# Performance work log

Measured on AMD Instinct MI355X. Metric: run time of the kernel, lower is better.

## Reference

```python
import jax, jax.numpy as jnp
import numpy as np

Q = 32          # latent position dim; state vs = [v, s] has dim 2Q
N = 131072      # batch of ODE states
H = 50          # BNN hidden width (n_hidden=50 in source)
STEPS = 16      # fixed-step Euler steps (dense time grid)
DT = 0.1        # dt default from forward()
LN_EPS = 1e-5


def setup_inputs() -> dict:
    key = jax.random.key(0)
    ks = jax.random.split(key, 6)
    d = 2 * Q
    # weights scaled by 1/sqrt(fan_in) so Euler integration stays stable
    return {
        "z0": jax.random.normal(ks[0], (N, d), jnp.float32),
        "logp0": jax.random.normal(ks[1], (N,), jnp.float32),
        "W1": jax.random.normal(ks[2], (d, H), jnp.float32) / np.sqrt(d).astype(np.float32),
        "b1": jnp.zeros((H,), jnp.float32),
        "g1": jnp.ones((H,), jnp.float32),
        "be1": jnp.zeros((H,), jnp.float32),
        "W2": jax.random.normal(ks[3], (H, H), jnp.float32) / np.sqrt(H).astype(np.float32),
        "b2": jnp.zeros((H,), jnp.float32),
        "g2": jnp.ones((H,), jnp.float32),
        "be2": jnp.zeros((H,), jnp.float32),
        "W3": jax.random.normal(ks[4], (H, Q), jnp.float32) / np.sqrt(H).astype(np.float32),
        "b3": jnp.zeros((Q,), jnp.float32),
    }


def _layernorm(x, g, b):
    m = jnp.mean(x, axis=-1, keepdims=True)
    v = jnp.mean((x - m) ** 2, axis=-1, keepdims=True)
    return (x - m) * jax.lax.rsqrt(v + LN_EPS) * g + b


def reference(z0, logp0, W1, b1, g1, be1, W2, b2, g2, be2, W3, b3):
    d = z0.shape[1]
    q = d // 2

    def f(vs):  # BNN dynamics: [N, 2q] -> [N, q]
        h = jax.nn.celu(_layernorm(vs @ W1 + b1, g1, be1))
        h = jax.nn.celu(_layernorm(h @ W2 + b2, g2, be2))
        return h @ W3 + b3

    basis = jnp.eye(q, d, dtype=z0.dtype)  # [q, 2q] unit tangents in the velocity block

    def rhs(vs):
        dv = f(vs)          # dv/dt = f(vs)
        ds = vs[:, :q]      # ds/dt = v
        dvs = jnp.concatenate([dv, ds], axis=1)
        # trace of d(dv)/d(v) via q forward-mode JVPs (fused analogue of the
        # per-dim torch.autograd.grad loop in ode2vae_rhs)
        def jvp_i(e):
            _, t = jax.jvp(f, (vs,), (jnp.broadcast_to(e, vs.shape),))
            return t  # [N, q]
        tang = jax.vmap(jvp_i)(basis)        # [q, N, q]
        tr = jnp.einsum("ini->n", tang)      # sum_i d(dv_i)/d(v_i)
        return dvs, -tr

    def step(carry, _):
        vs, lp = carry
        dvs, dlp = rhs(vs)
        vs2 = vs + DT * dvs
        lp2 = lp + DT * dlp
        return (vs2, lp2), (vs2, lp2)

    _, (zt, lp) = jax.lax.scan(step, (z0, logp0), None, length=STEPS)
    # [STEPS, N, 2q+1]: trajectory states with log-density appended
    return jnp.concatenate([zt, lp[..., None]], axis=-1)
```

## Files before the change

kernel.cpp:

```cpp
#include <hip/hip_runtime.h>
#include <hip/hip_fp16.h>

#define NPART 131072
#define QDIM 32
#define DDIM 64
#define HDIM 50
#define STEPS 16
#define DT 0.1f
#define LN_EPS 1e-5f
#define INV_H 0.02f
#define ODIM 65

#define WS_W1TH 0
#define WS_W2TH 1600
#define WS_UTH  3000
#define WS_MH   4400
#define WS_W3H  5800
#define WS_JV   6600
#define WS_HV   6800
#define WS_TOT  7000

#define LT_W2TH 0
#define LT_UTH  1400
#define LT_TOT  2800

#define SLOT_FLOATS (HDIM * 256)
#define LDS_FLOATS  (SLOT_FLOATS + LT_TOT)

typedef float f4a __attribute__((ext_vector_type(4)));
typedef float f4u __attribute__((ext_vector_type(4), aligned(4)));
typedef unsigned int u32;
typedef _Float16 h2f __attribute__((ext_vector_type(2)));

__device__ __forceinline__ h2f as_h2(u32 x) { h2f r; __builtin_memcpy(&r, &x, 4); return r; }
__device__ __forceinline__ u32 h2bits(float a, float b) {
    h2f p; p[0] = (_Float16)a; p[1] = (_Float16)b;
    u32 r; __builtin_memcpy(&r, &p, 4); return r;
}
__device__ __forceinline__ h2f mk_h2(float a, float b) {
    h2f p; p[0] = (_Float16)a; p[1] = (_Float16)b; return p;
}

#if __has_builtin(__builtin_amdgcn_fdot2)
#define FDOT2(a, b, c) __builtin_amdgcn_fdot2((a), (b), (c), false)
#else
#define FDOT2(a, b, c) ((float)(a)[0] * (float)(b)[0] + ((float)(a)[1] * (float)(b)[1] + (c)))
#endif

__global__ void ode2vae_setup(const float* __restrict__ W1,
                              const float* __restrict__ W2,
                              const float* __restrict__ W3,
                              const float* __restrict__ b1, const float* __restrict__ g1,
                              const float* __restrict__ be1,
                              const float* __restrict__ b2, const float* __restrict__ g2,
                              const float* __restrict__ be2,
                              float* __restrict__ ws)
{
    const int tid = threadIdx.x;
    u32* wsu = (u32*)ws;
    for (int i = tid; i < WS_TOT; i += 256) wsu[i] = 0u;
    __syncthreads();
    for (int idx = tid; idx < HDIM * 32; idx += 256) {
        const int h = idx / 32, k = idx % 32;
        wsu[WS_W1TH + h * 32 + k] = h2bits(W1[(2 * k) * HDIM + h], W1[(2 * k + 1) * HDIM + h]);
    }
    for (int idx = tid; idx < HDIM * 25; idx += 256) {
        const int j = idx / 25, k = idx % 25;
        float w2p[2], up[2], mp[2];
        #pragma unroll
        for (int s_ = 0; s_ < 2; ++s_) {
            const int h = 2 * k + s_;
            float u = 0.f;
            #pragma unroll
            for (int i = 0; i < QDIM; ++i)
                u = fmaf(W1[i * HDIM + h], W3[j * QDIM + i], u);
            const float w2 = W2[h * HDIM + j];
            float rs = 0.f;
            for (int jj = 0; jj < HDIM; ++jj) rs += W2[h * HDIM + jj];
            w2p[s_] = w2; up[s_] = u; mp[s_] = u * (w2 - INV_H * rs);
        }
        wsu[WS_W2TH + j * 28 + k] = h2bits(w2p[0], w2p[1]);
        wsu[WS_UTH  + j * 28 + k] = h2bits(up[0], up[1]);
        wsu[WS_MH   + j * 28 + k] = h2bits(mp[0], mp[1]);
    }
    for (int idx = tid; idx < HDIM * 16; idx += 256) {
        const int j = idx / 16, k = idx % 16;
        wsu[WS_W3H + j * 16 + k] = h2bits(W3[j * QDIM + 2 * k], W3[j * QDIM + 2 * k + 1]);
    }
    if (tid < HDIM) {
        float acc = 0.f;
        #pragma unroll
        for (int i = 0; i < QDIM; ++i) {
            float rs1 = 0.f;
            for (int h = 0; h < HDIM; ++h) rs1 += W1[i * HDIM + h];
            acc = fmaf(rs1, W3[tid * QDIM + i], acc);
        }
        ws[WS_JV + tid * 4 + 0] = g2[tid];
        ws[WS_JV + tid * 4 + 1] = be2[tid];
        ws[WS_JV + tid * 4 + 2] = b2[tid];
        ws[WS_JV + tid * 4 + 3] = acc;
        ws[WS_HV + tid * 4 + 0] = b1[tid];
        ws[WS_HV + tid * 4 + 1] = g1[tid];
        ws[WS_HV + tid * 4 + 2] = be1[tid];
        ws[WS_HV + tid * 4 + 3] = 0.f;
    }
}

#define DOT64(res, rowp, P)                                           \
    {                                                                 \
        float q0 = 0.f, q1 = 0.f, q2 = 0.f, q3 = 0.f;                 \
        const uint4* R_ = (const uint4*)(rowp);                       \
        _Pragma("unroll")                                             \
        for (int c_ = 0; c_ < 8; ++c_) {                              \
            const uint4 u_ = R_[c_];                                  \
            q0 = FDOT2(as_h2(u_.x), (P)[4*c_ + 0], q0);               \
            q1 = FDOT2(as_h2(u_.y), (P)[4*c_ + 1], q1);               \
            q2 = FDOT2(as_h2(u_.z), (P)[4*c_ + 2], q2);               \
            q3 = FDOT2(as_h2(u_.w), (P)[4*c_ + 3], q3);               \
        }                                                             \
        res = (q0 + q1) + (q2 + q3);                                  \
    }
#define DOT56(res, rowp, P)                                           \
    {                                                                 \
        float q0 = 0.f, q1 = 0.f, q2 = 0.f, q3 = 0.f;                 \
        const uint4* R_ = (const uint4*)(rowp);                       \
        _Pragma("unroll")                                             \
        for (int c_ = 0; c_ < 7; ++c_) {                              \
            const uint4 u_ = R_[c_];                                  \
            q0 = FDOT2(as_h2(u_.x), (P)[4*c_ + 0], q0);               \
            q1 = FDOT2(as_h2(u_.y), (P)[4*c_ + 1], q1);               \
            q2 = FDOT2(as_h2(u_.z), (P)[4*c_ + 2], q2);               \
            q3 = FDOT2(as_h2(u_.w), (P)[4*c_ + 3], q3);               \
        }                                                             \
        res = (q0 + q1) + (q2 + q3);                                  \
    }

#define LDROW7(RB, SRC) { const uint4* S_ = (const uint4*)(SRC);      \
    _Pragma("unroll") for (int c_ = 0; c_ < 7; ++c_) RB[c_] = S_[c_]; }
#define LDROW4(RB, SRC) { const uint4* S_ = (const uint4*)(SRC);      \
    _Pragma("unroll") for (int c_ = 0; c_ < 4; ++c_) RB[c_] = S_[c_]; }

#define PKDOT_RB(res, RB, P)                                          \
    {                                                                 \
        h2f a0 = mk_h2(0.f, 0.f), a1_ = a0;                           \
        _Pragma("unroll")                                             \
        for (int c_ = 0; c_ < 7; ++c_) {                              \
            a0  = as_h2(RB[c_].x) * (P)[4*c_ + 0] + a0;               \
            a1_ = as_h2(RB[c_].y) * (P)[4*c_ + 1] + a1_;              \
            a0  = as_h2(RB[c_].z) * (P)[4*c_ + 2] + a0;               \
            a1_ = as_h2(RB[c_].w) * (P)[4*c_ + 3] + a1_;              \
        }                                                             \
        a0 = a0 + a1_;                                                \
        res = (float)a0[0] + (float)a0[1];                            \
    }

#define PKDOT_SAX_RB(res, RB, PA, ys, D)                              \
    {                                                                 \
        h2f a0 = mk_h2(0.f, 0.f), a1_ = a0;                           \
        _Pragma("unroll")                                             \
        for (int c_ = 0; c_ < 7; ++c_) {                              \
            const h2f x_ = as_h2(RB[c_].x), y_ = as_h2(RB[c_].y);     \
            const h2f z_ = as_h2(RB[c_].z), w_ = as_h2(RB[c_].w);     \
            a0  = x_ * (PA)[4*c_ + 0] + a0;                           \
            (D)[4*c_ + 0] = x_ * (ys) + (D)[4*c_ + 0];                \
            a1_ = y_ * (PA)[4*c_ + 1] + a1_;                          \
            (D)[4*c_ + 1] = y_ * (ys) + (D)[4*c_ + 1];                \
            a0  = z_ * (PA)[4*c_ + 2] + a0;                           \
            (D)[4*c_ + 2] = z_ * (ys) + (D)[4*c_ + 2];                \
            a1_ = w_ * (PA)[4*c_ + 3] + a1_;                          \
            (D)[4*c_ + 3] = w_ * (ys) + (D)[4*c_ + 3];                \
        }                                                             \
        a0 = a0 + a1_;                                                \
        res = (float)a0[0] + (float)a0[1];                            \
    }

#define PK2DOT_SAX_RB(rA, rB, RB, PA, PB, xs, D)                      \
    {                                                                 \
        h2f aA = mk_h2(0.f, 0.f), aB = aA;                            \
        _Pragma("unroll")                                             \
        for (int c_ = 0; c_ < 7; ++c_) {                              \
            const h2f x_ = as_h2(RB[c_].x), y_ = as_h2(RB[c_].y);     \
            const h2f z_ = as_h2(RB[c_].z), w_ = as_h2(RB[c_].w);     \
            aA = x_ * (PA)[4*c_ + 0] + aA;                            \
            aB = x_ * (PB)[4*c_ + 0] + aB;                            \
            (D)[4*c_ + 0] = x_ * (xs) + (D)[4*c_ + 0];                \
            aA = y_ * (PA)[4*c_ + 1] + aA;                            \
            aB = y_ * (PB)[4*c_ + 1] + aB;                            \
            (D)[4*c_ + 1] = y_ * (xs) + (D)[4*c_ + 1];                \
            aA = z_ * (PA)[4*c_ + 2] + aA;                            \
            aB = z_ * (PB)[4*c_ + 2] + aB;                            \
            (D)[4*c_ + 2] = z_ * (xs) + (D)[4*c_ + 2];                \
            aA = w_ * (PA)[4*c_ + 3] + aA;                            \
            aB = w_ * (PB)[4*c_ + 3] + aB;                            \
            (D)[4*c_ + 3] = w_ * (xs) + (D)[4*c_ + 3];                \
        }                                                             \
        rA = (float)aA[0] + (float)aA[1];                             \
        rB = (float)aB[0] + (float)aB[1];                             \
    }

#define SAXPY_RB4(RB, sh, D)                                          \
    {                                                                 \
        _Pragma("unroll")                                             \
        for (int c_ = 0; c_ < 4; ++c_) {                              \
            (D)[4*c_ + 0] = as_h2(RB[c_].x) * (sh) + (D)[4*c_ + 0];   \
            (D)[4*c_ + 1] = as_h2(RB[c_].y) * (sh) + (D)[4*c_ + 1];   \
            (D)[4*c_ + 2] = as_h2(RB[c_].z) * (sh) + (D)[4*c_ + 2];   \
            (D)[4*c_ + 3] = as_h2(RB[c_].w) * (sh) + (D)[4*c_ + 3];   \
        }                                                             \
    }

__global__ __launch_bounds__(256, 2)
void ode2vae_main(const float* __restrict__ z0, const float* __restrict__ logp0,
                  const float* __restrict__ b3,
                  const float* __restrict__ wsc,
                  float* out)
{
    __shared__ float lds[LDS_FLOATS];
    const int tid = threadIdx.x;
    const int n = blockIdx.x * 256 + tid;

    {
        const u32* src = (const u32*)wsc;
        u32* dst = (u32*)(lds + SLOT_FLOATS);
        for (int i = tid; i < 1400; i += 256) dst[LT_W2TH + i] = src[WS_W2TH + i];
        for (int i = tid; i < 1400; i += 256) dst[LT_UTH + i]  = src[WS_UTH + i];
    }
    __syncthreads();

    float* const L = lds + tid;
    const u32* LW2TH = (const u32*)(lds + SLOT_FLOATS) + LT_W2TH;
    const u32* LUTH  = (const u32*)(lds + SLOT_FLOATS) + LT_UTH;
    const u32* GW1TH = (const u32*)wsc + WS_W1TH;
    const u32* GMH   = (const u32*)wsc + WS_MH;
    const u32* GW3H  = (const u32*)wsc + WS_W3H;
    const f4a* GJV   = (const f4a*)(wsc + WS_JV);
    const f4a* GHV   = (const f4a*)(wsc + WS_HV);

    float lp = logp0[n];
    const float* const zrow0 = z0 + (size_t)n * DDIM;

    for (int s = 0; s < STEPS; ++s) {
        float* const odst = out + ((size_t)s * NPART + (size_t)n) * ODIM;
        const float* const zprev = (s == 0) ? zrow0
            : (out + ((size_t)(s - 1) * NPART + (size_t)n) * ODIM);

        float zq[QDIM], zs[QDIM];
        #pragma unroll
        for (int k = 0; k < 8; ++k) {
            f4u v = *(const f4u*)(zprev + 4 * k);
            zq[4*k] = v[0]; zq[4*k+1] = v[1]; zq[4*k+2] = v[2]; zq[4*k+3] = v[3];
        }
        #pragma unroll
        for (int k = 0; k < 8; ++k) {
            f4u v = *(const f4u*)(zprev + QDIM + 4 * k);
            zs[4*k] = v[0]; zs[4*k+1] = v[1]; zs[4*k+2] = v[2]; zs[4*k+3] = v[3];
        }
        h2f zp[32];
        #pragma unroll
        for (int k = 0; k < 16; ++k) zp[k] = mk_h2(zq[2*k], zq[2*k+1]);
        #pragma unroll
        for (int k = 0; k < 16; ++k) zp[16 + k] = mk_h2(zs[2*k], zs[2*k+1]);

        float m1a = 0.f, v1a = 0.f;
        #pragma unroll 1
        for (int h = 0; h < HDIM; ++h) {
            float a1h;
            DOT64(a1h, GW1TH + h * 32, zp);
            const f4a hv = GHV[h];
            a1h += hv[0];
            L[h * 256] = a1h;
            m1a += a1h;
            v1a = fmaf(a1h, a1h, v1a);
        }
        #pragma unroll
        for (int k = 0; k < QDIM; ++k) zs[k] = fmaf(DT, zq[k], zs[k]);
        #pragma unroll
        for (int k = 0; k < 8; ++k) {
            f4u v = {zs[4*k], zs[4*k+1], zs[4*k+2], zs[4*k+3]};
            *(f4u*)(odst + QDIM + 4 * k) = v;
        }
        const float m1 = m1a * INV_H;
        float var1 = v1a * INV_H - m1 * m1;
        var1 = var1 > 0.f ? var1 : 0.f;
        const float r1 = rsqrtf(var1 + LN_EPS);

        h2f xh1p[28], hhp[28], w1vp[28], w1xp[28];
        #pragma unroll
        for (int hp = 0; hp < 25; ++hp) {
            const float xa = (L[(2*hp) * 256] - m1) * r1;
            const float xb = (L[(2*hp + 1) * 256] - m1) * r1;
            const f4a hva = GHV[2*hp], hvb = GHV[2*hp + 1];
            const float ya = fmaf(xa, hva[1], hva[2]);
            const float yb = fmaf(xb, hvb[1], hvb[2]);
            const float ea = __expf(ya), eb = __expf(yb);
            const float ca = (ya > 0.f) ? ya : (ea - 1.f);
            const float cb = (yb > 0.f) ? yb : (eb - 1.f);
            const float wa = ((ya > 0.f) ? 1.f : ea) * (hva[1] * r1);
            const float wb = ((yb > 0.f) ? 1.f : eb) * (hvb[1] * r1);
            xh1p[hp] = mk_h2(xa, xb);
            hhp[hp]  = mk_h2(ca, cb);
            w1vp[hp] = mk_h2(wa, wb);
            w1xp[hp] = mk_h2(wa * xa, wb * xb);
        }
        #pragma unroll
        for (int hp = 25; hp < 28; ++hp) {
            xh1p[hp] = mk_h2(0.f, 0.f); hhp[hp] = mk_h2(0.f, 0.f);
            w1vp[hp] = mk_h2(0.f, 0.f); w1xp[hp] = mk_h2(0.f, 0.f);
        }

        float m2a = 0.f, v2a = 0.f;
        #pragma unroll 1
        for (int j = 0; j < HDIM; ++j) {
            float a2j;
            DOT56(a2j, LW2TH + j * 28, hhp);
            const f4a jv = GJV[j];
            a2j += jv[2];
            L[j * 256] = a2j;
            m2a += a2j;
            v2a = fmaf(a2j, a2j, v2a);
        }
        const float m2 = m2a * INV_H;
        float var2 = v2a * INV_H - m2 * m2;
        var2 = var2 > 0.f ? var2 : 0.f;
        const float r2 = rsqrtf(var2 + LN_EPS);

        h2f duyp[28], php[28];
        #pragma unroll
        for (int k = 0; k < 28; ++k) { duyp[k] = mk_h2(0.f, 0.f); php[k] = mk_h2(0.f, 0.f); }
        h2f dvp[16];
        #pragma unroll
        for (int k = 0; k < 16; ++k) dvp[k] = mk_h2(0.f, 0.f);
        float suA = 0.f, syA = 0.f, tuA = 0.f, tyA = 0.f;
        float A2a = 0.f, A2b = 0.f, A2c = 0.f;
        float A3a = 0.f, A3b = 0.f, A3c = 0.f;
        float T1A = 0.f;
        #pragma unroll 1
        for (int j = 0; j < HDIM; ++j) {
            const float x2 = (L[j * 256] - m2) * r2;
            const f4a jv = GJV[j];
            const float y = fmaf(x2, jv[0], jv[1]);
            const float e = __expf(y);
            const float w2vj = ((y > 0.f) ? 1.f : e) * (jv[0] * r2);
            const float h2v = (y > 0.f) ? y : (e - 1.f);

            uint4 RU[7];
            LDROW7(RU, LUTH + j * 28);
            const float y3 = x2 * w2vj;
            const h2f y3h = mk_h2(y3, y3);
            float t;
            PKDOT_SAX_RB(t, RU, xh1p, y3h, duyp);

            uint4 RW[7];
            LDROW7(RW, LW2TH + j * 28);
            const h2f x2h = mk_h2(x2, x2);
            float cS2, cS3;
            PK2DOT_SAX_RB(cS2, cS3, RW, w1vp, w1xp, x2h, php);

            uint4 RM[7];
            LDROW7(RM, GMH + j * 28);
            float cTA;
            PKDOT_RB(cTA, RM, w1vp);

            uint4 R3[4];
            LDROW4(R3, GW3H + j * 16);
            const h2f hb = mk_h2(h2v, h2v);
            SAXPY_RB4(R3, hb, dvp);

            const float svw = jv[3] * w2vj;
            const float tw  = w2vj * t;
            suA += svw; syA = fmaf(svw, x2, syA);
            tuA += tw;  tyA = fmaf(tw, x2, tyA);
            A2a = fmaf(svw, cS2, A2a); A2b += cS2; A2c = fmaf(x2, cS2, A2c);
            A3a = fmaf(tw,  cS3, A3a); A3b += cS3; A3c = fmaf(x2, cS3, A3c);
            T1A = fmaf(w2vj, cTA, T1A);
        }

        float zq2[QDIM];
        #pragma unroll
        for (int k = 0; k < 8; ++k) {
            f4u v = *(const f4u*)(zprev + 4 * k);
            zq2[4*k] = v[0]; zq2[4*k+1] = v[1]; zq2[4*k+2] = v[2]; zq2[4*k+3] = v[3];
        }

        const float suH = suA * INV_H, syH = syA * INV_H;
        const float tuH = tuA * INV_H, tyH = tyA * INV_H;
        const float S2 = A2a - suH * A2b - syH * A2c;
        const float S3 = A3a - tuH * A3b - tyH * A3c;
        float T1c;
        {
            h2f acc0 = mk_h2(0.f, 0.f), acc1 = acc0;
            #pragma unroll
            for (int k = 0; k < 28; k += 2) {
                acc0 = (w1vp[k] * duyp[k]) * php[k] + acc0;
                acc1 = (w1vp[k+1] * duyp[k+1]) * php[k+1] + acc1;
            }
            acc0 = acc0 + acc1;
            T1c = (float)acc0[0] + (float)acc0[1];
        }
        const float tr = T1A - (T1c + S2 + S3) * INV_H;

        lp = fmaf(-DT, tr, lp);
        #pragma unroll
        for (int k = 0; k < 16; ++k) {
            const float da = (float)dvp[k][0] + b3[2*k];
            const float db = (float)dvp[k][1] + b3[2*k + 1];
            zq2[2*k]     = fmaf(DT, da, zq2[2*k]);
            zq2[2*k + 1] = fmaf(DT, db, zq2[2*k + 1]);
        }
        #pragma unroll
        for (int k = 0; k < 8; ++k) {
            f4u v = {zq2[4*k], zq2[4*k+1], zq2[4*k+2], zq2[4*k+3]};
            *(f4u*)(odst + 4 * k) = v;
        }
        odst[DDIM] = lp;
    }
}

extern "C" void kernel_launch(void* const* d_in, const int* in_sizes, int n_in,
                              void* d_out, int out_size, void* d_ws, size_t ws_size,
                              hipStream_t stream)
{
    const float* z0    = (const float*)d_in[0];
    const float* logp0 = (const float*)d_in[1];
    const float* W1    = (const float*)d_in[2];
    const float* b1    = (const float*)d_in[3];
    const float* g1    = (const float*)d_in[4];
    const float* be1   = (const float*)d_in[5];
    const float* W2    = (const float*)d_in[6];
    const float* b2    = (const float*)d_in[7];
    const float* g2    = (const float*)d_in[8];
    const float* be2   = (const float*)d_in[9];
    const float* W3    = (const float*)d_in[10];
    const float* b3    = (const float*)d_in[11];
    float* out = (float*)d_out;
    float* ws  = (float*)d_ws;

    hipLaunchKernelGGL(ode2vae_setup, dim3(1), dim3(256), 0, stream,
                       W1, W2, W3, b1, g1, be1, b2, g2, be2, ws);
    hipLaunchKernelGGL(ode2vae_main, dim3(NPART / 256), dim3(256), 0, stream,
                       z0, logp0, b3, ws, out);
}
```

Before: 1.347 ms.

## Pack per-thread LDS activations to fp16 pairs and move U matrix to global

The per-thread LDS scratch for layer activations now stores two fp16 values per 32-bit slot, halving its footprint. The U weight matrix is read from global (cached) memory instead of LDS, leaving only W2 in shared memory. The hidden loops are unrolled by two to match the packed layout. Less LDS per block can allow more resident blocks, but rounding pre-LayerNorm activations to fp16 loses precision and adds extra global or cache traffic for U.

```diff
diff --git a/kernel.cpp b/kernel.cpp
--- a/kernel.cpp
+++ b/kernel.cpp
@@ -20,12 +20,9 @@
 #define WS_HV   6800
 #define WS_TOT  7000
 
-#define LT_W2TH 0
-#define LT_UTH  1400
-#define LT_TOT  2800
-
-#define SLOT_FLOATS (HDIM * 256)
-#define LDS_FLOATS  (SLOT_FLOATS + LT_TOT)
+#define SLOT_U32   (25 * 256)
+#define LT_W2TH    SLOT_U32
+#define LDS_U32    (SLOT_U32 + 1400)
 
 typedef float f4a __attribute__((ext_vector_type(4)));
 typedef float f4u __attribute__((ext_vector_type(4), aligned(4)));
@@ -209,28 +206,61 @@
         }                                                             \
     }
 
+#define FUSED_BODY(JIDX, X2)                                          \
+    {                                                                 \
+        const f4a jv = GJV[JIDX];                                     \
+        const float y = fmaf((X2), jv[0], jv[1]);                     \
+        const float e = __expf(y);                                    \
+        const float w2vj = ((y > 0.f) ? 1.f : e) * (jv[0] * r2);      \
+        const float h2v = (y > 0.f) ? y : (e - 1.f);                  \
+        uint4 RU[7];                                                  \
+        LDROW7(RU, GUTH + (JIDX) * 28);                               \
+        const float y3 = (X2) * w2vj;                                 \
+        const h2f y3h = mk_h2(y3, y3);                                \
+        float t;                                                      \
+        PKDOT_SAX_RB(t, RU, xh1p, y3h, duyp);                         \
+        uint4 RW[7];                                                  \
+        LDROW7(RW, LW2TH + (JIDX) * 28);                              \
+        const h2f x2h = mk_h2((X2), (X2));                            \
+        float cS2, cS3;                                               \
+        PK2DOT_SAX_RB(cS2, cS3, RW, w1vp, w1xp, x2h, php);            \
+        uint4 RM[7];                                                  \
+        LDROW7(RM, GMH + (JIDX) * 28);                                \
+        float cTA;                                                    \
+        PKDOT_RB(cTA, RM, w1vp);                                      \
+        uint4 R3[4];                                                  \
+        LDROW4(R3, GW3H + (JIDX) * 16);                               \
+        const h2f hb = mk_h2(h2v, h2v);                               \
+        SAXPY_RB4(R3, hb, dvp);                                       \
+        const float svw = jv[3] * w2vj;                               \
+        const float tw  = w2vj * t;                                   \
+        suA += svw; syA = fmaf(svw, (X2), syA);                       \
+        tuA += tw;  tyA = fmaf(tw, (X2), tyA);                        \
+        A2a = fmaf(svw, cS2, A2a); A2b += cS2; A2c = fmaf((X2), cS2, A2c); \
+        A3a = fmaf(tw,  cS3, A3a); A3b += cS3; A3c = fmaf((X2), cS3, A3c); \
+        T1A = fmaf(w2vj, cTA, T1A);                                   \
+    }
+
 __global__ __launch_bounds__(256, 2)
 void ode2vae_main(const float* __restrict__ z0, const float* __restrict__ logp0,
                   const float* __restrict__ b3,
                   const float* __restrict__ wsc,
                   float* out)
 {
-    __shared__ float lds[LDS_FLOATS];
+    __shared__ u32 ldsU[LDS_U32];
     const int tid = threadIdx.x;
     const int n = blockIdx.x * 256 + tid;
 
     {
         const u32* src = (const u32*)wsc;
-        u32* dst = (u32*)(lds + SLOT_FLOATS);
-        for (int i = tid; i < 1400; i += 256) dst[LT_W2TH + i] = src[WS_W2TH + i];
-        for (int i = tid; i < 1400; i += 256) dst[LT_UTH + i]  = src[WS_UTH + i];
+        for (int i = tid; i < 1400; i += 256) ldsU[LT_W2TH + i] = src[WS_W2TH + i];
     }
     __syncthreads();
 
-    float* const L = lds + tid;
-    const u32* LW2TH = (const u32*)(lds + SLOT_FLOATS) + LT_W2TH;
-    const u32* LUTH  = (const u32*)(lds + SLOT_FLOATS) + LT_UTH;
+    u32* const Lp = ldsU + tid;
+    const u32* LW2TH = ldsU + LT_W2TH;
     const u32* GW1TH = (const u32*)wsc + WS_W1TH;
+    const u32* GUTH  = (const u32*)wsc + WS_UTH;
     const u32* GMH   = (const u32*)wsc + WS_MH;
     const u32* GW3H  = (const u32*)wsc + WS_W3H;
     const f4a* GJV   = (const f4a*)(wsc + WS_JV);
@@ -263,14 +293,16 @@
 
         float m1a = 0.f, v1a = 0.f;
         #pragma unroll 1
-        for (int h = 0; h < HDIM; ++h) {
-            float a1h;
-            DOT64(a1h, GW1TH + h * 32, zp);
-            const f4a hv = GHV[h];
-            a1h += hv[0];
-            L[h * 256] = a1h;
-            m1a += a1h;
-            v1a = fmaf(a1h, a1h, v1a);
+        for (int h = 0; h < HDIM; h += 2) {
+            float a1a, a1b;
+            DOT64(a1a, GW1TH + h * 32, zp);
+            DOT64(a1b, GW1TH + (h + 1) * 32, zp);
+            a1a += GHV[h][0];
+            a1b += GHV[h + 1][0];
+            Lp[(h >> 1) * 256] = h2bits(a1a, a1b);
+            m1a += a1a + a1b;
+            v1a = fmaf(a1a, a1a, v1a);
+            v1a = fmaf(a1b, a1b, v1a);
         }
         #pragma unroll
         for (int k = 0; k < QDIM; ++k) zs[k] = fmaf(DT, zq[k], zs[k]);
@@ -287,8 +319,9 @@
         h2f xh1p[28], hhp[28], w1vp[28], w1xp[28];
         #pragma unroll
         for (int hp = 0; hp < 25; ++hp) {
-            const float xa = (L[(2*hp) * 256] - m1) * r1;
-            const float xb = (L[(2*hp + 1) * 256] - m1) * r1;
+            const h2f ap = as_h2(Lp[hp * 256]);
+            const float xa = ((float)ap[0] - m1) * r1;
+            const float xb = ((float)ap[1] - m1) * r1;
             const f4a hva = GHV[2*hp], hvb = GHV[2*hp + 1];
             const float ya = fmaf(xa, hva[1], hva[2]);
             const float yb = fmaf(xb, hvb[1], hvb[2]);
@@ -310,14 +343,16 @@
 
         float m2a = 0.f, v2a = 0.f;
         #pragma unroll 1
-        for (int j = 0; j < HDIM; ++j) {
-            float a2j;
-            DOT56(a2j, LW2TH + j * 28, hhp);
-            const f4a jv = GJV[j];
-            a2j += jv[2];
-            L[j * 256] = a2j;
-            m2a += a2j;
-            v2a = fmaf(a2j, a2j, v2a);
+        for (int j = 0; j < HDIM; j += 2) {
+            float a2a, a2b;
+            DOT56(a2a, LW2TH + j * 28, hhp);
+            DOT56(a2b, LW2TH + (j + 1) * 28, hhp);
+            a2a += GJV[j][2];
+            a2b += GJV[j + 1][2];
+            Lp[(j >> 1) * 256] = h2bits(a2a, a2b);
+            m2a += a2a + a2b;
+            v2a = fmaf(a2a, a2a, v2a);
+            v2a = fmaf(a2b, a2b, v2a);
         }
         const float m2 = m2a * INV_H;
         float var2 = v2a * INV_H - m2 * m2;
@@ -335,44 +370,12 @@
         float A3a = 0.f, A3b = 0.f, A3c = 0.f;
         float T1A = 0.f;
         #pragma unroll 1
-        for (int j = 0; j < HDIM; ++j) {
-            const float x2 = (L[j * 256] - m2) * r2;
-            const f4a jv = GJV[j];
-            const float y = fmaf(x2, jv[0], jv[1]);
-            const float e = __expf(y);
-            const float w2vj = ((y > 0.f) ? 1.f : e) * (jv[0] * r2);
-            const float h2v = (y > 0.f) ? y : (e - 1.f);
-
-            uint4 RU[7];
-            LDROW7(RU, LUTH + j * 28);
-            const float y3 = x2 * w2vj;
-            const h2f y3h = mk_h2(y3, y3);
-            float t;
-            PKDOT_SAX_RB(t, RU, xh1p, y3h, duyp);
-
-            uint4 RW[7];
-            LDROW7(RW, LW2TH + j * 28);
-            const h2f x2h = mk_h2(x2, x2);
-            float cS2, cS3;
-            PK2DOT_SAX_RB(cS2, cS3, RW, w1vp, w1xp, x2h, php);
-
-            uint4 RM[7];
-            LDROW7(RM, GMH + j * 28);
-            float cTA;
-            PKDOT_RB(cTA, RM, w1vp);
-
-            uint4 R3[4];
-            LDROW4(R3, GW3H + j * 16);
-            const h2f hb = mk_h2(h2v, h2v);
-            SAXPY_RB4(R3, hb, dvp);
-
-            const float svw = jv[3] * w2vj;
-            const float tw  = w2vj * t;
-            suA += svw; syA = fmaf(svw, x2, syA);
-            tuA += tw;  tyA = fmaf(tw, x2, tyA);
-            A2a = fmaf(svw, cS2, A2a); A2b += cS2; A2c = fmaf(x2, cS2, A2c);
-            A3a = fmaf(tw,  cS3, A3a); A3b += cS3; A3c = fmaf(x2, cS3, A3c);
-            T1A = fmaf(w2vj, cTA, T1A);
+        for (int j = 0; j < HDIM; j += 2) {
+            const h2f pv = as_h2(Lp[(j >> 1) * 256]);
+            const float x2a = ((float)pv[0] - m2) * r2;
+            FUSED_BODY(j, x2a);
+            const float x2b = ((float)pv[1] - m2) * r2;
+            FUSED_BODY(j + 1, x2b);
         }
 
         float zq2[QDIM];
```

Result: slower. 1.570 ms (+16.6%).

## Split each ODE state across two threads with shuffle-reduced half dot products

Applied to the files above, without the earlier changes.

Each particle is now handled by a pair of lanes, each covering half of the hidden/input dimension (padded from 28 to 32 packed halves). Partial dot products are combined with lane-pair shuffles, and the two lanes split the output writes (velocity update vs position update). The setup kernel pads the weight tables to 32-word rows, and layer-1 bias/gain tables are staged in LDS. This halves per-thread register arrays to raise occupancy and doubles the thread count, at the cost of many extra shuffles per hidden unit and duplicated scalar LayerNorm/trace work on both lanes.

```diff
diff --git a/kernel.cpp b/kernel.cpp
--- a/kernel.cpp
+++ b/kernel.cpp
@@ -13,19 +13,17 @@
 
 #define WS_W1TH 0
 #define WS_W2TH 1600
-#define WS_UTH  3000
-#define WS_MH   4400
-#define WS_W3H  5800
-#define WS_JV   6600
-#define WS_HV   6800
-#define WS_TOT  7000
-
-#define LT_W2TH 0
-#define LT_UTH  1400
-#define LT_TOT  2800
-
-#define SLOT_FLOATS (HDIM * 256)
-#define LDS_FLOATS  (SLOT_FLOATS + LT_TOT)
+#define WS_UTH  3200
+#define WS_MH   4800
+#define WS_W3H  6400
+#define WS_JV   7200
+#define WS_HV   7400
+#define WS_TOT  7656
+
+#define LT_W2T  6400
+#define LT_UT   8000
+#define LT_HV   9600
+#define LDS_FLOATS 9856
 
 typedef float f4a __attribute__((ext_vector_type(4)));
 typedef float f4u __attribute__((ext_vector_type(4), aligned(4)));
@@ -33,6 +31,7 @@
 typedef _Float16 h2f __attribute__((ext_vector_type(2)));
 
 __device__ __forceinline__ h2f as_h2(u32 x) { h2f r; __builtin_memcpy(&r, &x, 4); return r; }
+__device__ __forceinline__ u32 h2_bits(h2f p) { u32 r; __builtin_memcpy(&r, &p, 4); return r; }
 __device__ __forceinline__ u32 h2bits(float a, float b) {
     h2f p; p[0] = (_Float16)a; p[1] = (_Float16)b;
     u32 r; __builtin_memcpy(&r, &p, 4); return r;
@@ -61,31 +60,33 @@
     for (int i = tid; i < WS_TOT; i += 256) wsu[i] = 0u;
     __syncthreads();
     for (int idx = tid; idx < HDIM * 32; idx += 256) {
-        const int h = idx / 32, k = idx % 32;
-        wsu[WS_W1TH + h * 32 + k] = h2bits(W1[(2 * k) * HDIM + h], W1[(2 * k + 1) * HDIM + h]);
-    }
-    for (int idx = tid; idx < HDIM * 25; idx += 256) {
-        const int j = idx / 25, k = idx % 25;
+        const int h = idx >> 5, k = idx & 31, d = 2 * k;
+        wsu[WS_W1TH + idx] = h2bits(W1[d * HDIM + h], W1[(d + 1) * HDIM + h]);
+    }
+    for (int idx = tid; idx < HDIM * 32; idx += 256) {
+        const int j = idx >> 5, k = idx & 31;
         float w2p[2], up[2], mp[2];
         #pragma unroll
-        for (int s_ = 0; s_ < 2; ++s_) {
-            const int h = 2 * k + s_;
-            float u = 0.f;
-            #pragma unroll
-            for (int i = 0; i < QDIM; ++i)
-                u = fmaf(W1[i * HDIM + h], W3[j * QDIM + i], u);
-            const float w2 = W2[h * HDIM + j];
-            float rs = 0.f;
-            for (int jj = 0; jj < HDIM; ++jj) rs += W2[h * HDIM + jj];
-            w2p[s_] = w2; up[s_] = u; mp[s_] = u * (w2 - INV_H * rs);
-        }
-        wsu[WS_W2TH + j * 28 + k] = h2bits(w2p[0], w2p[1]);
-        wsu[WS_UTH  + j * 28 + k] = h2bits(up[0], up[1]);
-        wsu[WS_MH   + j * 28 + k] = h2bits(mp[0], mp[1]);
+        for (int t2 = 0; t2 < 2; ++t2) {
+            const int h = 2 * k + t2;
+            if (h < HDIM) {
+                float u = 0.f;
+                #pragma unroll
+                for (int i = 0; i < QDIM; ++i)
+                    u = fmaf(W1[i * HDIM + h], W3[j * QDIM + i], u);
+                const float w2 = W2[h * HDIM + j];
+                float rs = 0.f;
+                for (int jj = 0; jj < HDIM; ++jj) rs += W2[h * HDIM + jj];
+                w2p[t2] = w2; up[t2] = u; mp[t2] = u * (w2 - INV_H * rs);
+            } else { w2p[t2] = 0.f; up[t2] = 0.f; mp[t2] = 0.f; }
+        }
+        wsu[WS_W2TH + idx] = h2bits(w2p[0], w2p[1]);
+        wsu[WS_UTH  + idx] = h2bits(up[0], up[1]);
+        wsu[WS_MH   + idx] = h2bits(mp[0], mp[1]);
     }
     for (int idx = tid; idx < HDIM * 16; idx += 256) {
-        const int j = idx / 16, k = idx % 16;
-        wsu[WS_W3H + j * 16 + k] = h2bits(W3[j * QDIM + 2 * k], W3[j * QDIM + 2 * k + 1]);
+        const int j = idx >> 4, k = idx & 15;
+        wsu[WS_W3H + idx] = h2bits(W3[j * QDIM + 2 * k], W3[j * QDIM + 2 * k + 1]);
     }
     if (tid < HDIM) {
         float acc = 0.f;
@@ -106,108 +107,56 @@
     }
 }
 
-#define DOT64(res, rowp, P)                                           \
-    {                                                                 \
-        float q0 = 0.f, q1 = 0.f, q2 = 0.f, q3 = 0.f;                 \
-        const uint4* R_ = (const uint4*)(rowp);                       \
-        _Pragma("unroll")                                             \
-        for (int c_ = 0; c_ < 8; ++c_) {                              \
-            const uint4 u_ = R_[c_];                                  \
-            q0 = FDOT2(as_h2(u_.x), (P)[4*c_ + 0], q0);               \
-            q1 = FDOT2(as_h2(u_.y), (P)[4*c_ + 1], q1);               \
-            q2 = FDOT2(as_h2(u_.z), (P)[4*c_ + 2], q2);               \
-            q3 = FDOT2(as_h2(u_.w), (P)[4*c_ + 3], q3);               \
-        }                                                             \
-        res = (q0 + q1) + (q2 + q3);                                  \
-    }
-#define DOT56(res, rowp, P)                                           \
-    {                                                                 \
-        float q0 = 0.f, q1 = 0.f, q2 = 0.f, q3 = 0.f;                 \
-        const uint4* R_ = (const uint4*)(rowp);                       \
-        _Pragma("unroll")                                             \
-        for (int c_ = 0; c_ < 7; ++c_) {                              \
-            const uint4 u_ = R_[c_];                                  \
-            q0 = FDOT2(as_h2(u_.x), (P)[4*c_ + 0], q0);               \
-            q1 = FDOT2(as_h2(u_.y), (P)[4*c_ + 1], q1);               \
-            q2 = FDOT2(as_h2(u_.z), (P)[4*c_ + 2], q2);               \
-            q3 = FDOT2(as_h2(u_.w), (P)[4*c_ + 3], q3);               \
-        }                                                             \
-        res = (q0 + q1) + (q2 + q3);                                  \
-    }
-
-#define LDROW7(RB, SRC) { const uint4* S_ = (const uint4*)(SRC);      \
-    _Pragma("unroll") for (int c_ = 0; c_ < 7; ++c_) RB[c_] = S_[c_]; }
-#define LDROW4(RB, SRC) { const uint4* S_ = (const uint4*)(SRC);      \
+#define LD4(RB, SRC) { const uint4* S_ = (const uint4*)(SRC); \
     _Pragma("unroll") for (int c_ = 0; c_ < 4; ++c_) RB[c_] = S_[c_]; }
-
-#define PKDOT_RB(res, RB, P)                                          \
-    {                                                                 \
-        h2f a0 = mk_h2(0.f, 0.f), a1_ = a0;                           \
-        _Pragma("unroll")                                             \
-        for (int c_ = 0; c_ < 7; ++c_) {                              \
-            a0  = as_h2(RB[c_].x) * (P)[4*c_ + 0] + a0;               \
-            a1_ = as_h2(RB[c_].y) * (P)[4*c_ + 1] + a1_;              \
-            a0  = as_h2(RB[c_].z) * (P)[4*c_ + 2] + a0;               \
-            a1_ = as_h2(RB[c_].w) * (P)[4*c_ + 3] + a1_;              \
-        }                                                             \
-        a0 = a0 + a1_;                                                \
-        res = (float)a0[0] + (float)a0[1];                            \
-    }
-
-#define PKDOT_SAX_RB(res, RB, PA, ys, D)                              \
-    {                                                                 \
-        h2f a0 = mk_h2(0.f, 0.f), a1_ = a0;                           \
-        _Pragma("unroll")                                             \
-        for (int c_ = 0; c_ < 7; ++c_) {                              \
-            const h2f x_ = as_h2(RB[c_].x), y_ = as_h2(RB[c_].y);     \
-            const h2f z_ = as_h2(RB[c_].z), w_ = as_h2(RB[c_].w);     \
-            a0  = x_ * (PA)[4*c_ + 0] + a0;                           \
-            (D)[4*c_ + 0] = x_ * (ys) + (D)[4*c_ + 0];                \
-            a1_ = y_ * (PA)[4*c_ + 1] + a1_;                          \
-            (D)[4*c_ + 1] = y_ * (ys) + (D)[4*c_ + 1];                \
-            a0  = z_ * (PA)[4*c_ + 2] + a0;                           \
-            (D)[4*c_ + 2] = z_ * (ys) + (D)[4*c_ + 2];                \
-            a1_ = w_ * (PA)[4*c_ + 3] + a1_;                          \
-            (D)[4*c_ + 3] = w_ * (ys) + (D)[4*c_ + 3];                \
-        }                                                             \
-        a0 = a0 + a1_;                                                \
-        res = (float)a0[0] + (float)a0[1];                            \
-    }
-
-#define PK2DOT_SAX_RB(rA, rB, RB, PA, PB, xs, D)                      \
-    {                                                                 \
-        h2f aA = mk_h2(0.f, 0.f), aB = aA;                            \
-        _Pragma("unroll")                                             \
-        for (int c_ = 0; c_ < 7; ++c_) {                              \
-            const h2f x_ = as_h2(RB[c_].x), y_ = as_h2(RB[c_].y);     \
-            const h2f z_ = as_h2(RB[c_].z), w_ = as_h2(RB[c_].w);     \
-            aA = x_ * (PA)[4*c_ + 0] + aA;                            \
-            aB = x_ * (PB)[4*c_ + 0] + aB;                            \
-            (D)[4*c_ + 0] = x_ * (xs) + (D)[4*c_ + 0];                \
-            aA = y_ * (PA)[4*c_ + 1] + aA;                            \
-            aB = y_ * (PB)[4*c_ + 1] + aB;                            \
-            (D)[4*c_ + 1] = y_ * (xs) + (D)[4*c_ + 1];                \
-            aA = z_ * (PA)[4*c_ + 2] + aA;                            \
-            aB = z_ * (PB)[4*c_ + 2] + aB;                            \
-            (D)[4*c_ + 2] = z_ * (xs) + (D)[4*c_ + 2];                \
-            aA = w_ * (PA)[4*c_ + 3] + aA;                            \
-            aB = w_ * (PB)[4*c_ + 3] + aB;                            \
-            (D)[4*c_ + 3] = w_ * (xs) + (D)[4*c_ + 3];                \
-        }                                                             \
-        rA = (float)aA[0] + (float)aA[1];                             \
-        rB = (float)aB[0] + (float)aB[1];                             \
-    }
-
-#define SAXPY_RB4(RB, sh, D)                                          \
-    {                                                                 \
-        _Pragma("unroll")                                             \
-        for (int c_ = 0; c_ < 4; ++c_) {                              \
-            (D)[4*c_ + 0] = as_h2(RB[c_].x) * (sh) + (D)[4*c_ + 0];   \
-            (D)[4*c_ + 1] = as_h2(RB[c_].y) * (sh) + (D)[4*c_ + 1];   \
-            (D)[4*c_ + 2] = as_h2(RB[c_].z) * (sh) + (D)[4*c_ + 2];   \
-            (D)[4*c_ + 3] = as_h2(RB[c_].w) * (sh) + (D)[4*c_ + 3];   \
-        }                                                             \
-    }
+#define LD2(RB, SRC) { const uint4* S_ = (const uint4*)(SRC); \
+    _Pragma("unroll") for (int c_ = 0; c_ < 2; ++c_) RB[c_] = S_[c_]; }
+
+#define DOT16F(res, RB, P) { float q0=0.f,q1=0.f,q2=0.f,q3=0.f; \
+    _Pragma("unroll") for (int c_ = 0; c_ < 4; ++c_) { const uint4 u_ = RB[c_]; \
+        q0 = FDOT2(as_h2(u_.x), (P)[4*c_+0], q0); \
+        q1 = FDOT2(as_h2(u_.y), (P)[4*c_+1], q1); \
+        q2 = FDOT2(as_h2(u_.z), (P)[4*c_+2], q2); \
+        q3 = FDOT2(as_h2(u_.w), (P)[4*c_+3], q3); } \
+    res = (q0 + q1) + (q2 + q3); }
+
+#define PKDOT16(res, RB, P) { h2f a0 = mk_h2(0.f,0.f), a1_ = a0; \
+    _Pragma("unroll") for (int c_ = 0; c_ < 4; ++c_) { \
+        a0  = as_h2(RB[c_].x) * (P)[4*c_+0] + a0; \
+        a1_ = as_h2(RB[c_].y) * (P)[4*c_+1] + a1_; \
+        a0  = as_h2(RB[c_].z) * (P)[4*c_+2] + a0; \
+        a1_ = as_h2(RB[c_].w) * (P)[4*c_+3] + a1_; } \
+    a0 = a0 + a1_; res = (float)a0[0] + (float)a0[1]; }
+
+#define PKDOT_SAX16(res, RB, PA, ys, D) { h2f a0 = mk_h2(0.f,0.f), a1_ = a0; \
+    _Pragma("unroll") for (int c_ = 0; c_ < 4; ++c_) { \
+        const h2f x_ = as_h2(RB[c_].x), y_ = as_h2(RB[c_].y); \
+        const h2f z_ = as_h2(RB[c_].z), w_ = as_h2(RB[c_].w); \
+        a0  = x_ * (PA)[4*c_+0] + a0; (D)[4*c_+0] = x_ * (ys) + (D)[4*c_+0]; \
+        a1_ = y_ * (PA)[4*c_+1] + a1_;(D)[4*c_+1] = y_ * (ys) + (D)[4*c_+1]; \
+        a0  = z_ * (PA)[4*c_+2] + a0; (D)[4*c_+2] = z_ * (ys) + (D)[4*c_+2]; \
+        a1_ = w_ * (PA)[4*c_+3] + a1_;(D)[4*c_+3] = w_ * (ys) + (D)[4*c_+3]; } \
+    a0 = a0 + a1_; res = (float)a0[0] + (float)a0[1]; }
+
+#define PK2DOT_SAX16(rA, rB_, RB, PA, PB, xs, D) { h2f aA = mk_h2(0.f,0.f), aB = aA; \
+    _Pragma("unroll") for (int c_ = 0; c_ < 4; ++c_) { \
+        const h2f x_ = as_h2(RB[c_].x), y_ = as_h2(RB[c_].y); \
+        const h2f z_ = as_h2(RB[c_].z), w_ = as_h2(RB[c_].w); \
+        aA = x_ * (PA)[4*c_+0] + aA; aB = x_ * (PB)[4*c_+0] + aB; \
+        (D)[4*c_+0] = x_ * (xs) + (D)[4*c_+0]; \
+        aA = y_ * (PA)[4*c_+1] + aA; aB = y_ * (PB)[4*c_+1] + aB; \
+        (D)[4*c_+1] = y_ * (xs) + (D)[4*c_+1]; \
+        aA = z_ * (PA)[4*c_+2] + aA; aB = z_ * (PB)[4*c_+2] + aB; \
+        (D)[4*c_+2] = z_ * (xs) + (D)[4*c_+2]; \
+        aA = w_ * (PA)[4*c_+3] + aA; aB = w_ * (PB)[4*c_+3] + aB; \
+        (D)[4*c_+3] = w_ * (xs) + (D)[4*c_+3]; } \
+    rA = (float)aA[0] + (float)aA[1]; rB_ = (float)aB[0] + (float)aB[1]; }
+
+#define SAXPY8(RB, sh, D) { _Pragma("unroll") for (int c_ = 0; c_ < 2; ++c_) { \
+        (D)[4*c_+0] = as_h2(RB[c_].x) * (sh) + (D)[4*c_+0]; \
+        (D)[4*c_+1] = as_h2(RB[c_].y) * (sh) + (D)[4*c_+1]; \
+        (D)[4*c_+2] = as_h2(RB[c_].z) * (sh) + (D)[4*c_+2]; \
+        (D)[4*c_+3] = as_h2(RB[c_].w) * (sh) + (D)[4*c_+3]; } }
 
 __global__ __launch_bounds__(256, 2)
 void ode2vae_main(const float* __restrict__ z0, const float* __restrict__ logp0,
@@ -217,154 +166,151 @@
 {
     __shared__ float lds[LDS_FLOATS];
     const int tid = threadIdx.x;
-    const int n = blockIdx.x * 256 + tid;
+    const int par = tid & 1;
+    const int pid = tid >> 1;
+    const int n = blockIdx.x * 128 + pid;
 
     {
         const u32* src = (const u32*)wsc;
-        u32* dst = (u32*)(lds + SLOT_FLOATS);
-        for (int i = tid; i < 1400; i += 256) dst[LT_W2TH + i] = src[WS_W2TH + i];
-        for (int i = tid; i < 1400; i += 256) dst[LT_UTH + i]  = src[WS_UTH + i];
+        u32* ldsu = (u32*)lds;
+        for (int i = tid; i < 1600; i += 256) ldsu[LT_W2T + i] = src[WS_W2TH + i];
+        for (int i = tid; i < 1600; i += 256) ldsu[LT_UT + i]  = src[WS_UTH + i];
+        if (tid < 256) lds[LT_HV + tid] = wsc[WS_HV + tid];
     }
     __syncthreads();
 
-    float* const L = lds + tid;
-    const u32* LW2TH = (const u32*)(lds + SLOT_FLOATS) + LT_W2TH;
-    const u32* LUTH  = (const u32*)(lds + SLOT_FLOATS) + LT_UTH;
-    const u32* GW1TH = (const u32*)wsc + WS_W1TH;
-    const u32* GMH   = (const u32*)wsc + WS_MH;
-    const u32* GW3H  = (const u32*)wsc + WS_W3H;
-    const f4a* GJV   = (const f4a*)(wsc + WS_JV);
-    const f4a* GHV   = (const f4a*)(wsc + WS_HV);
+    float* const SL = lds + pid;
+    const u32* LW2T = (const u32*)lds + LT_W2T;
+    const u32* LUT  = (const u32*)lds + LT_UT;
+    const f4a* LHV  = (const f4a*)(lds + LT_HV);
+    const u32* GW1  = (const u32*)wsc + WS_W1TH;
+    const u32* GM   = (const u32*)wsc + WS_MH;
+    const u32* GW3  = (const u32*)wsc + WS_W3H;
+    const f4a* GJV  = (const f4a*)(wsc + WS_JV);
 
     float lp = logp0[n];
     const float* const zrow0 = z0 + (size_t)n * DDIM;
+    const int hbase = par * 32;
 
     for (int s = 0; s < STEPS; ++s) {
         float* const odst = out + ((size_t)s * NPART + (size_t)n) * ODIM;
         const float* const zprev = (s == 0) ? zrow0
             : (out + ((size_t)(s - 1) * NPART + (size_t)n) * ODIM);
 
-        float zq[QDIM], zs[QDIM];
-        #pragma unroll
-        for (int k = 0; k < 8; ++k) {
-            f4u v = *(const f4u*)(zprev + 4 * k);
-            zq[4*k] = v[0]; zq[4*k+1] = v[1]; zq[4*k+2] = v[2]; zq[4*k+3] = v[3];
-        }
-        #pragma unroll
-        for (int k = 0; k < 8; ++k) {
-            f4u v = *(const f4u*)(zprev + QDIM + 4 * k);
-            zs[4*k] = v[0]; zs[4*k+1] = v[1]; zs[4*k+2] = v[2]; zs[4*k+3] = v[3];
-        }
-        h2f zp[32];
-        #pragma unroll
-        for (int k = 0; k < 16; ++k) zp[k] = mk_h2(zq[2*k], zq[2*k+1]);
-        #pragma unroll
-        for (int k = 0; k < 16; ++k) zp[16 + k] = mk_h2(zs[2*k], zs[2*k+1]);
-
+        h2f zh[16];
+        {
+            const float* zsrc = zprev + par * QDIM;
+            #pragma unroll
+            for (int k = 0; k < 8; ++k) {
+                f4u v = *(const f4u*)(zsrc + 4 * k);
+                zh[2*k]     = mk_h2(v[0], v[1]);
+                zh[2*k + 1] = mk_h2(v[2], v[3]);
+            }
+        }
         float m1a = 0.f, v1a = 0.f;
         #pragma unroll 1
         for (int h = 0; h < HDIM; ++h) {
-            float a1h;
-            DOT64(a1h, GW1TH + h * 32, zp);
-            const f4a hv = GHV[h];
-            a1h += hv[0];
-            L[h * 256] = a1h;
+            uint4 RB[4];
+            LD4(RB, GW1 + h * 32 + par * 16);
+            float half;
+            DOT16F(half, RB, zh);
+            float a1h = half + __shfl_xor(half, 1, 64);
+            a1h += LHV[h][0];
+            if (par == 0) SL[h * 128] = a1h;
             m1a += a1h;
             v1a = fmaf(a1h, a1h, v1a);
-        }
-        #pragma unroll
-        for (int k = 0; k < QDIM; ++k) zs[k] = fmaf(DT, zq[k], zs[k]);
-        #pragma unroll
-        for (int k = 0; k < 8; ++k) {
-            f4u v = {zs[4*k], zs[4*k+1], zs[4*k+2], zs[4*k+3]};
-            *(f4u*)(odst + QDIM + 4 * k) = v;
         }
         const float m1 = m1a * INV_H;
         float var1 = v1a * INV_H - m1 * m1;
         var1 = var1 > 0.f ? var1 : 0.f;
         const float r1 = rsqrtf(var1 + LN_EPS);
 
-        h2f xh1p[28], hhp[28], w1vp[28], w1xp[28];
-        #pragma unroll
-        for (int hp = 0; hp < 25; ++hp) {
-            const float xa = (L[(2*hp) * 256] - m1) * r1;
-            const float xb = (L[(2*hp + 1) * 256] - m1) * r1;
-            const f4a hva = GHV[2*hp], hvb = GHV[2*hp + 1];
-            const float ya = fmaf(xa, hva[1], hva[2]);
-            const float yb = fmaf(xb, hvb[1], hvb[2]);
-            const float ea = __expf(ya), eb = __expf(yb);
-            const float ca = (ya > 0.f) ? ya : (ea - 1.f);
-            const float cb = (yb > 0.f) ? yb : (eb - 1.f);
-            const float wa = ((ya > 0.f) ? 1.f : ea) * (hva[1] * r1);
-            const float wb = ((yb > 0.f) ? 1.f : eb) * (hvb[1] * r1);
+        h2f xh1p[16], hhp[16], w1vp[16], w1xp[16];
+        #pragma unroll
+        for (int hp = 0; hp < 16; ++hp) {
+            const int h0 = hbase + 2 * hp;
+            float xa = 0.f, xb = 0.f, ca = 0.f, cb = 0.f, wa = 0.f, wb = 0.f;
+            if (h0 < HDIM) {
+                const float aa = SL[h0 * 128];
+                const float ab = SL[h0 * 128 + 128];
+                const f4a hva = LHV[h0], hvb = LHV[h0 + 1];
+                xa = (aa - m1) * r1; xb = (ab - m1) * r1;
+                const float ya = fmaf(xa, hva[1], hva[2]);
+                const float yb = fmaf(xb, hvb[1], hvb[2]);
+                const float ea = __expf(ya), eb = __expf(yb);
+                ca = (ya > 0.f) ? ya : (ea - 1.f);
+                cb = (yb > 0.f) ? yb : (eb - 1.f);
+                wa = ((ya > 0.f) ? 1.f : ea) * (hva[1] * r1);
+                wb = ((yb > 0.f) ? 1.f : eb) * (hvb[1] * r1);
+            }
             xh1p[hp] = mk_h2(xa, xb);
             hhp[hp]  = mk_h2(ca, cb);
             w1vp[hp] = mk_h2(wa, wb);
             w1xp[hp] = mk_h2(wa * xa, wb * xb);
         }
-        #pragma unroll
-        for (int hp = 25; hp < 28; ++hp) {
-            xh1p[hp] = mk_h2(0.f, 0.f); hhp[hp] = mk_h2(0.f, 0.f);
-            w1vp[hp] = mk_h2(0.f, 0.f); w1xp[hp] = mk_h2(0.f, 0.f);
-        }
 
         float m2a = 0.f, v2a = 0.f;
         #pragma unroll 1
         for (int j = 0; j < HDIM; ++j) {
-            float a2j;
-            DOT56(a2j, LW2TH + j * 28, hhp);
-            const f4a jv = GJV[j];
-            a2j += jv[2];
-            L[j * 256] = a2j;
-            m2a += a2j;
-            v2a = fmaf(a2j, a2j, v2a);
+            uint4 RB[4];
+            LD4(RB, LW2T + j * 32 + par * 16);
+            float half;
+            DOT16F(half, RB, hhp);
+            float a2 = half + __shfl_xor(half, 1, 64);
+            a2 += GJV[j][2];
+            if (par == 0) SL[j * 128] = a2;
+            m2a += a2;
+            v2a = fmaf(a2, a2, v2a);
         }
         const float m2 = m2a * INV_H;
         float var2 = v2a * INV_H - m2 * m2;
         var2 = var2 > 0.f ? var2 : 0.f;
         const float r2 = rsqrtf(var2 + LN_EPS);
 
-        h2f duyp[28], php[28];
-        #pragma unroll
-        for (int k = 0; k < 28; ++k) { duyp[k] = mk_h2(0.f, 0.f); php[k] = mk_h2(0.f, 0.f); }
-        h2f dvp[16];
-        #pragma unroll
-        for (int k = 0; k < 16; ++k) dvp[k] = mk_h2(0.f, 0.f);
+        h2f duyp[16], php[16], dvp[8];
+        #pragma unroll
+        for (int k = 0; k < 16; ++k) { duyp[k] = mk_h2(0.f, 0.f); php[k] = mk_h2(0.f, 0.f); }
+        #pragma unroll
+        for (int k = 0; k < 8; ++k) dvp[k] = mk_h2(0.f, 0.f);
         float suA = 0.f, syA = 0.f, tuA = 0.f, tyA = 0.f;
         float A2a = 0.f, A2b = 0.f, A2c = 0.f;
         float A3a = 0.f, A3b = 0.f, A3c = 0.f;
         float T1A = 0.f;
         #pragma unroll 1
         for (int j = 0; j < HDIM; ++j) {
-            const float x2 = (L[j * 256] - m2) * r2;
+            const float x2 = (SL[j * 128] - m2) * r2;
             const f4a jv = GJV[j];
             const float y = fmaf(x2, jv[0], jv[1]);
             const float e = __expf(y);
             const float w2vj = ((y > 0.f) ? 1.f : e) * (jv[0] * r2);
             const float h2v = (y > 0.f) ? y : (e - 1.f);
-
-            uint4 RU[7];
-            LDROW7(RU, LUTH + j * 28);
             const float y3 = x2 * w2vj;
+
+            uint4 RU[4];
+            LD4(RU, LUT + j * 32 + par * 16);
             const h2f y3h = mk_h2(y3, y3);
-            float t;
-            PKDOT_SAX_RB(t, RU, xh1p, y3h, duyp);
-
-            uint4 RW[7];
-            LDROW7(RW, LW2TH + j * 28);
+            float tH;
+            PKDOT_SAX16(tH, RU, xh1p, y3h, duyp);
+            const float t = tH + __shfl_xor(tH, 1, 64);
+
+            uint4 RW[4];
+            LD4(RW, LW2T + j * 32 + par * 16);
             const h2f x2h = mk_h2(x2, x2);
-            float cS2, cS3;
-            PK2DOT_SAX_RB(cS2, cS3, RW, w1vp, w1xp, x2h, php);
-
-            uint4 RM[7];
-            LDROW7(RM, GMH + j * 28);
-            float cTA;
-            PKDOT_RB(cTA, RM, w1vp);
-
-            uint4 R3[4];
-            LDROW4(R3, GW3H + j * 16);
+            float c2H, c3H;
+            PK2DOT_SAX16(c2H, c3H, RW, w1vp, w1xp, x2h, php);
+            const float cS2 = c2H + __shfl_xor(c2H, 1, 64);
+            const float cS3 = c3H + __shfl_xor(c3H, 1, 64);
+
+            uint4 RM[4];
+            LD4(RM, GM + j * 32 + par * 16);
+            float cTH;
+            PKDOT16(cTH, RM, w1vp);
+            const float cTA = cTH + __shfl_xor(cTH, 1, 64);
+
+            uint4 R3[2];
+            LD2(R3, GW3 + j * 16 + par * 8);
             const h2f hb = mk_h2(h2v, h2v);
-            SAXPY_RB4(R3, hb, dvp);
+            SAXPY8(R3, hb, dvp);
 
             const float svw = jv[3] * w2vj;
             const float tw  = w2vj * t;
@@ -375,44 +321,57 @@
             T1A = fmaf(w2vj, cTA, T1A);
         }
 
-        float zq2[QDIM];
-        #pragma unroll
-        for (int k = 0; k < 8; ++k) {
-            f4u v = *(const f4u*)(zprev + 4 * k);
-            zq2[4*k] = v[0]; zq2[4*k+1] = v[1]; zq2[4*k+2] = v[2]; zq2[4*k+3] = v[3];
-        }
-
+        float T1cH;
+        {
+            h2f acc0 = mk_h2(0.f, 0.f), acc1 = acc0;
+            #pragma unroll
+            for (int k = 0; k < 16; k += 2) {
+                acc0 = (w1vp[k] * duyp[k]) * php[k] + acc0;
+                acc1 = (w1vp[k+1] * duyp[k+1]) * php[k+1] + acc1;
+            }
+            acc0 = acc0 + acc1;
+            T1cH = (float)acc0[0] + (float)acc0[1];
+        }
+        const float T1c = T1cH + __shfl_xor(T1cH, 1, 64);
         const float suH = suA * INV_H, syH = syA * INV_H;
         const float tuH = tuA * INV_H, tyH = tyA * INV_H;
         const float S2 = A2a - suH * A2b - syH * A2c;
         const float S3 = A3a - tuH * A3b - tyH * A3c;
-        float T1c;
-        {
-            h2f acc0 = mk_h2(0.f, 0.f), acc1 = acc0;
+        const float tr = T1A - (T1c + S2 + S3) * INV_H;
+        lp = fmaf(-DT, tr, lp);
+
+        u32 odvb[8];
+        #pragma unroll
+        for (int k = 0; k < 8; ++k) odvb[k] = __shfl_xor(h2_bits(dvp[k]), 1, 64);
+
+        if (par == 0) {
             #pragma unroll
-            for (int k = 0; k < 28; k += 2) {
-                acc0 = (w1vp[k] * duyp[k]) * php[k] + acc0;
-                acc1 = (w1vp[k+1] * duyp[k+1]) * php[k+1] + acc1;
+            for (int k = 0; k < 8; ++k) {
+                f4u q = *(const f4u*)(zprev + 4 * k);
+                h2f dA_, dB_;
+                if (k < 4) { dA_ = dvp[2*k]; dB_ = dvp[2*k + 1]; }
+                else       { dA_ = as_h2(odvb[2*(k-4)]); dB_ = as_h2(odvb[2*(k-4) + 1]); }
+                f4u o;
+                o[0] = fmaf(DT, (float)dA_[0] + b3[4*k + 0], q[0]);
+                o[1] = fmaf(DT, (float)dA_[1] + b3[4*k + 1], q[1]);
+                o[2] = fmaf(DT, (float)dB_[0] + b3[4*k + 2], q[2]);
+                o[3] = fmaf(DT, (float)dB_[1] + b3[4*k + 3], q[3]);
+                *(f4u*)(odst + 4 * k) = o;
             }
-            acc0 = acc0 + acc1;
-            T1c = (float)acc0[0] + (float)acc0[1];
-        }
-        const float tr = T1A - (T1c + S2 + S3) * INV_H;
-
-        lp = fmaf(-DT, tr, lp);
-        #pragma unroll
-        for (int k = 0; k < 16; ++k) {
-            const float da = (float)dvp[k][0] + b3[2*k];
-            const float db = (float)dvp[k][1] + b3[2*k + 1];
-            zq2[2*k]     = fmaf(DT, da, zq2[2*k]);
-            zq2[2*k + 1] = fmaf(DT, db, zq2[2*k + 1]);
-        }
-        #pragma unroll
-        for (int k = 0; k < 8; ++k) {
-            f4u v = {zq2[4*k], zq2[4*k+1], zq2[4*k+2], zq2[4*k+3]};
-            *(f4u*)(odst + 4 * k) = v;
-        }
-        odst[DDIM] = lp;
+            odst[DDIM] = lp;
+        } else {
+            #pragma unroll
+            for (int k = 0; k < 8; ++k) {
+                f4u q  = *(const f4u*)(zprev + 4 * k);
+                f4u sv = *(const f4u*)(zprev + QDIM + 4 * k);
+                f4u o;
+                o[0] = fmaf(DT, q[0], sv[0]);
+                o[1] = fmaf(DT, q[1], sv[1]);
+                o[2] = fmaf(DT, q[2], sv[2]);
+                o[3] = fmaf(DT, q[3], sv[3]);
+                *(f4u*)(odst + QDIM + 4 * k) = o;
+            }
+        }
     }
 }
 
@@ -437,6 +396,6 @@
 
     hipLaunchKernelGGL(ode2vae_setup, dim3(1), dim3(256), 0, stream,
                        W1, W2, W3, b1, g1, be1, b2, g2, be2, ws);
-    hipLaunchKernelGGL(ode2vae_main, dim3(NPART / 256), dim3(256), 0, stream,
+    hipLaunchKernelGGL(ode2vae_main, dim3(NPART / 128), dim3(256), 0, stream,
                        z0, logp0, b3, ws, out);
 }
```

Result: slower. 2.319 ms (+72.2%).
